# Kernel optimization log

Hardware: AMD Instinct MI355X
Metric: run time of the kernel (lower is better)

The kernel has to match this reference:

```python
import jax, jax.numpy as jnp
from jax import lax
import numpy as np

DIM = 48
HEADS = 2
HIDDEN = 96  # int(dim * 2.0)
EPS_LN = 1e-5
EPS_NORM = 1e-12


def _ln(x, w, b):
    # WithBias LayerNorm over channel dim (dim=1 in NCHW == last dim in b,(hw),c)
    mu = jnp.mean(x, axis=1, keepdims=True)
    var = jnp.var(x, axis=1, keepdims=True)
    return (x - mu) / jnp.sqrt(var + EPS_LN) * w[None, :, None, None] + b[None, :, None, None]


def _conv1x1(x, w, b):
    # w: [O, C, 1, 1]
    return jnp.einsum('bchw,oc->bohw', x, w[:, :, 0, 0]) + b[None, :, None, None]


def _dwconv3(x, w, b):
    # w: [C, 1, 3, 3], groups=C
    y = lax.conv_general_dilated(x, w, (1, 1), 'SAME',
                                 feature_group_count=x.shape[1],
                                 dimension_numbers=('NCHW', 'OIHW', 'NCHW'))
    return y + b[None, :, None, None]


def _l2norm(x):
    n = jnp.sqrt(jnp.sum(x * x, axis=-1, keepdims=True))
    return x / jnp.maximum(n, EPS_NORM)


def setup_inputs() -> dict:
    key = jax.random.key(0)
    ks = jax.random.split(key, 12)
    s = 0.02
    inp = {
        'x': jax.random.normal(ks[0], (2, DIM, 64, 64), jnp.float32),
        'norm1_w': jnp.ones((DIM,), jnp.float32),
        'norm1_b': jnp.zeros((DIM,), jnp.float32),
        'qkv_w': jax.random.normal(ks[1], (DIM * 3, DIM, 1, 1), jnp.float32) * s,
        'qkv_b': jnp.zeros((DIM * 3,), jnp.float32),
        'qkvdw_w': jax.random.normal(ks[2], (DIM * 3, 1, 3, 3), jnp.float32) * s,
        'qkvdw_b': jnp.zeros((DIM * 3,), jnp.float32),
        'temperature': jnp.ones((HEADS, 1, 1), jnp.float32),
        'proj_w': jax.random.normal(ks[3], (DIM, DIM, 1, 1), jnp.float32) * s,
        'proj_b': jnp.zeros((DIM,), jnp.float32),
        'norm2_w': jnp.ones((DIM,), jnp.float32),
        'norm2_b': jnp.zeros((DIM,), jnp.float32),
        'fi_w': jax.random.normal(ks[4], (HIDDEN * 2, DIM, 1, 1), jnp.float32) * s,
        'fi_b': jnp.zeros((HIDDEN * 2,), jnp.float32),
        'fdw_w': jax.random.normal(ks[5], (HIDDEN * 2, 1, 3, 3), jnp.float32) * s,
        'fdw_b': jnp.zeros((HIDDEN * 2,), jnp.float32),
        'fo_w': jax.random.normal(ks[6], (DIM, HIDDEN, 1, 1), jnp.float32) * s,
        'fo_b': jnp.zeros((DIM,), jnp.float32),
    }
    return inp


def _block(x, norm1_w, norm1_b, qkv_w, qkv_b, qkvdw_w, qkvdw_b, temperature,
           proj_w, proj_b, norm2_w, norm2_b, fi_w, fi_b, fdw_w, fdw_b, fo_w, fo_b):
    b, c, h, w = x.shape
    n = h * w
    chead = c // HEADS
    # --- attention branch ---
    xn = _ln(x, norm1_w, norm1_b)
    qkv = _dwconv3(_conv1x1(xn, qkv_w, qkv_b), qkvdw_w, qkvdw_b)
    q, k, v = jnp.split(qkv, 3, axis=1)
    def to_heads(t):  # [b, heads*chead, h, w] -> [b, heads, n, chead]
        return t.reshape(b, HEADS, chead, n).transpose(0, 1, 3, 2)
    q, k, v = to_heads(q), to_heads(k), to_heads(v)
    q = _l2norm(q)
    k = _l2norm(k)
    attn = jnp.einsum('bhnc,bhmc->bhnm', q, k) * temperature[None]
    attn = jax.nn.softmax(attn, axis=-1)
    out = jnp.einsum('bhnm,bhmc->bhnc', attn, v)
    out = out.transpose(0, 1, 3, 2).reshape(b, c, h, w)
    x = x + _conv1x1(out, proj_w, proj_b)
    # --- ffn branch ---
    xn = _ln(x, norm2_w, norm2_b)
    y = _dwconv3(_conv1x1(xn, fi_w, fi_b), fdw_w, fdw_b)
    y1, y2 = jnp.split(y, 2, axis=1)
    y = jax.nn.gelu(y1, approximate=False) * y2
    x = x + _conv1x1(y, fo_w, fo_b)
    return x


def reference(x, norm1_w, norm1_b, qkv_w, qkv_b, qkvdw_w, qkvdw_b, temperature,
              proj_w, proj_b, norm2_w, norm2_b, fi_w, fi_b, fdw_w, fdw_b, fo_w, fo_b):
    return _block(x, norm1_w, norm1_b, qkv_w, qkv_b, qkvdw_w, qkvdw_b, temperature,
                  proj_w, proj_b, norm2_w, norm2_b, fi_w, fi_b, fdw_w, fdw_b, fo_w, fo_b)
```

## Files before the change

kernel.cpp:

```cpp
#include <hip/hip_runtime.h>
#include <hip/hip_bf16.h>
#include <math.h>

#define NPIX 4096
#define NB 2

typedef __attribute__((ext_vector_type(8))) short short8;
typedef __attribute__((ext_vector_type(4))) short short4s;
typedef __attribute__((ext_vector_type(4))) float floatx4;

static __device__ inline short f2bf(float f) {
    union { float f; unsigned u; } v; v.f = f;
    unsigned r = (v.u + 0x7FFFu + ((v.u >> 16) & 1u)) >> 16;
    return (short)r;
}
static __device__ inline float bf2f(short s) {
    union { unsigned u; float f; } v;
    v.u = ((unsigned)(unsigned short)s) << 16;
    return v.f;
}
static __device__ inline unsigned pk2(float a, float b) {
    __hip_bfloat162 pk = __float22bfloat162_rn(make_float2(a, b));
    return *(unsigned*)&pk;
}

__global__ void k_prepw(const float* __restrict__ qkvw, const float* __restrict__ fiw,
                        const float* __restrict__ fow, const float* __restrict__ projw,
                        short* __restrict__ qkvwbf, short* __restrict__ fiwbf,
                        short* __restrict__ fowbf, short* __restrict__ projwbf) {
    int idx = blockIdx.x * 256 + threadIdx.x;
    if (idx < 144 * 64) {
        int o = idx >> 6, c = idx & 63;
        qkvwbf[idx] = (c < 48) ? f2bf(qkvw[o * 48 + c]) : (short)0;
        return;
    }
    idx -= 144 * 64;
    if (idx < 192 * 64) {
        int o = idx >> 6, c = idx & 63;
        fiwbf[idx] = (c < 48) ? f2bf(fiw[o * 48 + c]) : (short)0;
        return;
    }
    idx -= 192 * 64;
    if (idx < 48 * 96) {
        fowbf[idx] = f2bf(fow[idx]);
        return;
    }
    idx -= 48 * 96;
    if (idx < 48 * 64) {
        int o = idx >> 6, c = idx & 63;
        int h = c >> 5, cc = c & 31;
        projwbf[idx] = (cc < 24) ? f2bf(projw[o * 48 + h * 24 + cc]) : (short)0;
    }
}

__global__ __launch_bounds__(256) void k_qkv_fused(
    const float* __restrict__ xin, const float* __restrict__ n1w, const float* __restrict__ n1b,
    const short* __restrict__ qkvwbf, const float* __restrict__ qkvb,
    const float* __restrict__ dww, const float* __restrict__ dwb,
    const float* __restrict__ temp,
    short* __restrict__ Qbf, short* __restrict__ Kbf, short* __restrict__ Vbf)
{
    int px0 = blockIdx.x * 16;
    int y = blockIdx.y, b = blockIdx.z;
    int t = threadIdx.x;
    int w = t >> 6, lane = t & 63, l15 = lane & 15, quad = lane >> 4;

    __shared__ __align__(16) short xn[64][72];
    __shared__ short qkv[64][148];
    __shared__ float q2[16][148];
    __shared__ float red[4][64], redq[4][64];
    __shared__ float muS[64], rsS[64];
    __shared__ float dwwS[1296], dwbS[144];
    __shared__ short vmask[64];

    for (int u = t; u < 1296; u += 256) dwwS[u] = dww[u];
    if (t < 144) dwbS[t] = dwb[t];

    int pp = t & 63, cg = t >> 6;
    int rr = pp / 18, ix = pp - rr * 18;
    int yy = y + rr - 1, xpx = px0 - 1 + ix;
    bool pv = (pp < 54) && ((unsigned)yy < 64u) && ((unsigned)xpx < 64u);
    if (cg == 0) vmask[pp] = pv ? (short)1 : (short)0;

    float v[12]; float s = 0.f, sq = 0.f;
    if (pv) {
        size_t pbase = (size_t)(yy * 64 + xpx);
#pragma unroll
        for (int j = 0; j < 12; j++) {
            float vv = xin[((size_t)b * 48 + cg * 12 + j) * NPIX + pbase];
            v[j] = vv; s += vv; sq += vv * vv;
        }
    } else {
#pragma unroll
        for (int j = 0; j < 12; j++) v[j] = 0.f;
    }
    red[cg][pp] = s; redq[cg][pp] = sq;
    __syncthreads();
    if (t < 64) {
        float ss = red[0][t] + red[1][t] + red[2][t] + red[3][t];
        float qq = redq[0][t] + redq[1][t] + redq[2][t] + redq[3][t];
        float mu = ss * (1.f / 48.f);
        float var = qq * (1.f / 48.f) - mu * mu;
        muS[t] = mu; rsS[t] = rsqrtf(var + 1e-5f);
    }
    __syncthreads();
    {
        float mu = muS[pp], rs = rsS[pp];
#pragma unroll
        for (int j = 0; j < 12; j++) {
            int c = cg * 12 + j;
            xn[pp][c] = f2bf((v[j] - mu) * rs * n1w[c] + n1b[c]);
        }
        short8 z8 = {};
        if (cg == 0) *(short8*)&xn[pp][48] = z8;
        else if (cg == 1) *(short8*)&xn[pp][56] = z8;
    }
    __syncthreads();
    floatx4 zf = {0.f, 0.f, 0.f, 0.f};
    for (int job = w; job < 36; job += 4) {
        int pt = job / 9, ot = job % 9;
        short8 a0 = *(const short8*)&xn[pt * 16 + l15][quad * 8];
        short8 a1 = *(const short8*)&xn[pt * 16 + l15][32 + quad * 8];
        const short* wb = qkvwbf + (ot * 16 + l15) * 64;
        short8 b0 = *(const short8*)(wb + quad * 8);
        short8 b1 = *(const short8*)(wb + 32 + quad * 8);
        floatx4 c = __builtin_amdgcn_mfma_f32_16x16x32_bf16(a0, b0, zf, 0, 0, 0);
        c = __builtin_amdgcn_mfma_f32_16x16x32_bf16(a1, b1, c, 0, 0, 0);
        int oc = ot * 16 + l15;
        float bi = qkvb[oc];
#pragma unroll
        for (int r = 0; r < 4; r++) {
            int opp = pt * 16 + quad * 4 + r;
            qkv[opp][oc] = vmask[opp] ? f2bf(c[r] + bi) : (short)0;
        }
    }
    __syncthreads();
    {
        int i = t & 15, g = t >> 4;
        for (int cc = 0; cc < 9; cc++) {
            int c = g * 9 + cc;
            const float* wp = dwwS + c * 9;
            float acc = dwbS[c];
#pragma unroll
            for (int dy = 0; dy < 3; dy++)
#pragma unroll
                for (int dx = 0; dx < 3; dx++)
                    acc += bf2f(qkv[dy * 18 + i + dx][c]) * wp[dy * 3 + dx];
            q2[i][c] = acc;
        }
    }
    __syncthreads();
    if (t < 128) {
        int i = t & 15, h = (t >> 4) & 1, sel = t >> 5;
        int n = y * 64 + px0 + i;
        int bh = b * 2 + h;
        if (sel < 2) {
            float vv2[24]; float ss = 0.f;
            int base = sel * 48 + h * 24;
#pragma unroll
            for (int c = 0; c < 24; c++) { vv2[c] = q2[i][base + c]; ss += vv2[c] * vv2[c]; }
            float sc = ((sel == 0) ? temp[h] : 1.f) / fmaxf(sqrtf(ss), 1e-12f);
            short qs[32];
#pragma unroll
            for (int c = 0; c < 24; c++) qs[c] = f2bf(vv2[c] * sc);
#pragma unroll
            for (int c = 24; c < 32; c++) qs[c] = 0;
            short* dst = ((sel == 0) ? Qbf : Kbf) + ((size_t)bh * NPIX + n) * 32;
#pragma unroll
            for (int i8 = 0; i8 < 4; i8++) {
                short8 st;
#pragma unroll
                for (int j = 0; j < 8; j++) st[j] = qs[i8 * 8 + j];
                *(short8*)(dst + i8 * 8) = st;
            }
        } else {
            int half = sel - 2;
            int r5 = n & 31;
            int pos = (r5 < 16) ? ((r5 >> 2) * 8 + (r5 & 3))
                                : (((r5 & 15) >> 2) * 8 + (r5 & 3) + 4);
            int vcol = (n & ~31) + pos;
#pragma unroll
            for (int cc = 0; cc < 12; cc++) {
                int c = half * 12 + cc;
                Vbf[((size_t)bh * 32 + c) * NPIX + vcol] = f2bf(q2[i][96 + h * 24 + c]);
            }
            if (half == 1) {
#pragma unroll
                for (int c = 24; c < 32; c++)
                    Vbf[((size_t)bh * 32 + c) * NPIX + vcol] = 0;
            }
        }
    }
}

__global__ __launch_bounds__(1024) void k_attn_mfma2(
    const short* __restrict__ Qbf, const short* __restrict__ Kbf,
    const short* __restrict__ Vbf, short* __restrict__ O)
{
    int qt = blockIdx.x, bh = blockIdx.y;
    int t = threadIdx.x;
    int tg = t & 255, g = t >> 8;
    int wloc = (t >> 6) & 3, lane = t & 63, l15 = lane & 15, quad = lane >> 4;

    __shared__ __align__(16) short tileK[4][2][64][40];
    __shared__ __align__(16) short tileV[4][2][32][72];
    __shared__ float Ocomb[4][64][33];
    __shared__ float Lcomb[4][64];

    int qrow0 = qt * 64 + wloc * 16;
    short8 bq = *(const short8*)(Qbf + ((size_t)bh * NPIX + qrow0 + l15) * 32 + quad * 8);

    int krow = tg >> 2, kseg = tg & 3;
    int vch = tg >> 3, vseg = tg & 7;
    const short* srcK = Kbf + ((size_t)bh * NPIX + krow) * 32 + kseg * 8;
    const short* srcV = Vbf + ((size_t)(bh * 32 + vch)) * NPIX + vseg * 8;

    int key0 = g * 1024;
    *(short8*)&tileK[g][0][krow][kseg * 8] = *(const short8*)(srcK + (size_t)key0 * 32);
    *(short8*)&tileV[g][0][vch][vseg * 8]  = *(const short8*)(srcV + key0);

    floatx4 zf = {0.f, 0.f, 0.f, 0.f};
    floatx4 o0 = zf, o1 = zf;
    float ls = 0.f;

    const int NKT = 16;
    for (int kt = 0; kt < NKT; kt++) {
        __syncthreads();
        int cur = kt & 1;
        short8 ldK = {}, ldV = {};
        if (kt < NKT - 1) {
            int kabs = key0 + (kt + 1) * 64;
            ldK = *(const short8*)(srcK + (size_t)kabs * 32);
            ldV = *(const short8*)(srcV + kabs);
        }
        short8 ka0 = *(const short8*)&tileK[g][cur][l15][quad * 8];
        short8 ka1 = *(const short8*)&tileK[g][cur][16 + l15][quad * 8];
        short8 ka2 = *(const short8*)&tileK[g][cur][32 + l15][quad * 8];
        short8 ka3 = *(const short8*)&tileK[g][cur][48 + l15][quad * 8];
        floatx4 s0 = __builtin_amdgcn_mfma_f32_16x16x32_bf16(ka0, bq, zf, 0, 0, 0);
        floatx4 s1 = __builtin_amdgcn_mfma_f32_16x16x32_bf16(ka1, bq, zf, 0, 0, 0);
        floatx4 s2 = __builtin_amdgcn_mfma_f32_16x16x32_bf16(ka2, bq, zf, 0, 0, 0);
        floatx4 s3 = __builtin_amdgcn_mfma_f32_16x16x32_bf16(ka3, bq, zf, 0, 0, 0);
        float e0[4], e1[4], e2[4], e3[4];
#pragma unroll
        for (int r = 0; r < 4; r++) {
            e0[r] = __expf(s0[r]); e1[r] = __expf(s1[r]);
            e2[r] = __expf(s2[r]); e3[r] = __expf(s3[r]);
            ls += (e0[r] + e1[r]) + (e2[r] + e3[r]);
        }
        short8 p01, p23;
        {
            unsigned* u01 = (unsigned*)&p01;
            unsigned* u23 = (unsigned*)&p23;
            u01[0] = pk2(e0[0], e0[1]); u01[1] = pk2(e0[2], e0[3]);
            u01[2] = pk2(e1[0], e1[1]); u01[3] = pk2(e1[2], e1[3]);
            u23[0] = pk2(e2[0], e2[1]); u23[1] = pk2(e2[2], e2[3]);
            u23[2] = pk2(e3[0], e3[1]); u23[3] = pk2(e3[2], e3[3]);
        }
        short8 va00 = *(const short8*)&tileV[g][cur][l15][quad * 8];
        short8 va01 = *(const short8*)&tileV[g][cur][l15][32 + quad * 8];
        short8 va10 = *(const short8*)&tileV[g][cur][16 + l15][quad * 8];
        short8 va11 = *(const short8*)&tileV[g][cur][16 + l15][32 + quad * 8];
        o0 = __builtin_amdgcn_mfma_f32_16x16x32_bf16(va00, p01, o0, 0, 0, 0);
        o0 = __builtin_amdgcn_mfma_f32_16x16x32_bf16(va01, p23, o0, 0, 0, 0);
        o1 = __builtin_amdgcn_mfma_f32_16x16x32_bf16(va10, p01, o1, 0, 0, 0);
        o1 = __builtin_amdgcn_mfma_f32_16x16x32_bf16(va11, p23, o1, 0, 0, 0);
        if (kt < NKT - 1) {
            *(short8*)&tileK[g][1 - cur][krow][kseg * 8] = ldK;
            *(short8*)&tileV[g][1 - cur][vch][vseg * 8]  = ldV;
        }
    }
    ls += __shfl_xor(ls, 16, 64);
    ls += __shfl_xor(ls, 32, 64);
    int qi = wloc * 16 + l15;
#pragma unroll
    for (int r = 0; r < 4; r++) {
        Ocomb[g][qi][quad * 4 + r]      = o0[r];
        Ocomb[g][qi][16 + quad * 4 + r] = o1[r];
    }
    if (quad == 0) Lcomb[g][qi] = ls;
    __syncthreads();
    {
        int qq = t >> 4, cp = t & 15;
        float l4 = Lcomb[0][qq] + Lcomb[1][qq] + Lcomb[2][qq] + Lcomb[3][qq];
        float inv = 1.f / l4;
        float sa = (Ocomb[0][qq][2 * cp] + Ocomb[1][qq][2 * cp] +
                    Ocomb[2][qq][2 * cp] + Ocomb[3][qq][2 * cp]) * inv;
        float sb = (Ocomb[0][qq][2 * cp + 1] + Ocomb[1][qq][2 * cp + 1] +
                    Ocomb[2][qq][2 * cp + 1] + Ocomb[3][qq][2 * cp + 1]) * inv;
        int b = bh >> 1, h = bh & 1;
        int n = qt * 64 + qq;
        *(unsigned*)(O + ((size_t)b * NPIX + n) * 64 + h * 32 + 2 * cp) = pk2(sa, sb);
    }
}

__global__ __launch_bounds__(256) void k_tail_fused(
    const float* __restrict__ xin, const short* __restrict__ O,
    const short* __restrict__ projwbf, const float* __restrict__ projb,
    const float* __restrict__ n2w, const float* __restrict__ n2b,
    const short* __restrict__ fiwbf, const float* __restrict__ fib,
    const float* __restrict__ fdww, const float* __restrict__ fdwb,
    const short* __restrict__ fowbf, const float* __restrict__ fob,
    float* __restrict__ out)
{
    int px0 = blockIdx.x * 16;
    int y = blockIdx.y, b = blockIdx.z;
    int t = threadIdx.x;
    int w = t >> 6, lane = t & 63, l15 = lane & 15, quad = lane >> 4;

    __shared__ float x1s[64][53];
    __shared__ __align__(16) short xn2[64][72];
    __shared__ short ypre[56][196];
    __shared__ __align__(16) short yv[16][104];
    __shared__ float red[4][64], redq[4][64];
    __shared__ float muS[64], rsS[64];
    __shared__ float fdwwS[1728], fdwbS[192];
    __shared__ short vmask[64];
    __shared__ int nidx[64];

    for (int u = t; u < 1728; u += 256) fdwwS[u] = fdww[u];
    if (t < 192) fdwbS[t] = fdwb[t];
    if (t < 64) {
        int rr = t / 18, ix = t - rr * 18;
        int yy = y + rr - 1, xpx = px0 - 1 + ix;
        bool pv = (t < 54) && ((unsigned)yy < 64u) && ((unsigned)xpx < 64u);
        vmask[t] = pv ? (short)1 : (short)0;
        int n = yy * 64 + xpx;
        n = n < 0 ? 0 : (n > 4095 ? 4095 : n);
        nidx[t] = n;
    }
    __syncthreads();

    floatx4 zf = {0.f, 0.f, 0.f, 0.f};
    for (int job = w; job < 12; job += 4) {
        int pt = job / 3, ot = job % 3;
        const short* oa = O + ((size_t)b * NPIX + nidx[pt * 16 + l15]) * 64;
        short8 a0 = *(const short8*)(oa + quad * 8);
        short8 a1 = *(const short8*)(oa + 32 + quad * 8);
        const short* wb = projwbf + (ot * 16 + l15) * 64;
        short8 b0 = *(const short8*)(wb + quad * 8);
        short8 b1 = *(const short8*)(wb + 32 + quad * 8);
        floatx4 c = __builtin_amdgcn_mfma_f32_16x16x32_bf16(a0, b0, zf, 0, 0, 0);
        c = __builtin_amdgcn_mfma_f32_16x16x32_bf16(a1, b1, c, 0, 0, 0);
        int oc = ot * 16 + l15;
        float bi = projb[oc];
#pragma unroll
        for (int r = 0; r < 4; r++) {
            int opp = pt * 16 + quad * 4 + r;
            x1s[opp][oc] = xin[((size_t)b * 48 + oc) * NPIX + nidx[opp]] + c[r] + bi;
        }
    }
    __syncthreads();
    int pp = t & 63, cg = t >> 6;
    {
        float v[12]; float s = 0.f, sq = 0.f;
#pragma unroll
        for (int j = 0; j < 12; j++) {
            float vv = x1s[pp][cg * 12 + j];
            v[j] = vv; s += vv; sq += vv * vv;
        }
        red[cg][pp] = s; redq[cg][pp] = sq;
        __syncthreads();
        if (t < 64) {
            float ss = red[0][t] + red[1][t] + red[2][t] + red[3][t];
            float qq = redq[0][t] + redq[1][t] + redq[2][t] + redq[3][t];
            float mu = ss * (1.f / 48.f);
            float var = qq * (1.f / 48.f) - mu * mu;
            muS[t] = mu; rsS[t] = rsqrtf(var + 1e-5f);
        }
        __syncthreads();
        float mu = muS[pp], rs = rsS[pp];
#pragma unroll
        for (int j = 0; j < 12; j++) {
            int c = cg * 12 + j;
            xn2[pp][c] = f2bf((v[j] - mu) * rs * n2w[c] + n2b[c]);
        }
        short8 z8 = {};
        if (cg == 0) *(short8*)&xn2[pp][48] = z8;
        else if (cg == 1) *(short8*)&xn2[pp][56] = z8;
    }
    __syncthreads();
    for (int job = w; job < 48; job += 4) {
        int pt = job / 12, ot = job % 12;
        short8 a0 = *(const short8*)&xn2[pt * 16 + l15][quad * 8];
        short8 a1 = *(const short8*)&xn2[pt * 16 + l15][32 + quad * 8];
        const short* wb = fiwbf + (ot * 16 + l15) * 64;
        short8 b0 = *(const short8*)(wb + quad * 8);
        short8 b1 = *(const short8*)(wb + 32 + quad * 8);
        floatx4 c = __builtin_amdgcn_mfma_f32_16x16x32_bf16(a0, b0, zf, 0, 0, 0);
        c = __builtin_amdgcn_mfma_f32_16x16x32_bf16(a1, b1, c, 0, 0, 0);
        int oc = ot * 16 + l15;
        float bi = fib[oc];
#pragma unroll
        for (int r = 0; r < 4; r++) {
            int opp = pt * 16 + quad * 4 + r;
            if (opp < 56) ypre[opp][oc] = vmask[opp] ? f2bf(c[r] + bi) : (short)0;
        }
    }
    __syncthreads();
    {
        int i = t & 15, gg = t >> 4;
        for (int cc = 0; cc < 6; cc++) {
            int c = gg * 6 + cc;
            const float* wp  = fdwwS + c * 9;
            const float* wp2 = fdwwS + (c + 96) * 9;
            float a = fdwbS[c], g2v = fdwbS[c + 96];
#pragma unroll
            for (int dy = 0; dy < 3; dy++)
#pragma unroll
                for (int dx = 0; dx < 3; dx++) {
                    int ppi = dy * 18 + i + dx;
                    a   += bf2f(ypre[ppi][c])      * wp[dy * 3 + dx];
                    g2v += bf2f(ypre[ppi][c + 96]) * wp2[dy * 3 + dx];
                }
            float ge = 0.5f * a * (1.f + erff(a * 0.70710678118654752f));
            yv[i][c] = f2bf(ge * g2v);
        }
        short8 z8 = {};
        if (gg == 0) *(short8*)&yv[i][96] = z8;
    }
    __syncthreads();
    if (w < 3) {
        floatx4 c = zf;
#pragma unroll
        for (int k = 0; k < 3; k++) {
            short8 a  = *(const short8*)&yv[l15][k * 32 + quad * 8];
            short8 bb = *(const short8*)(fowbf + (w * 16 + l15) * 96 + k * 32 + quad * 8);
            c = __builtin_amdgcn_mfma_f32_16x16x32_bf16(a, bb, c, 0, 0, 0);
        }
        int oc = w * 16 + l15;
        float bi = fob[oc];
#pragma unroll
        for (int r = 0; r < 4; r++) {
            int i = quad * 4 + r;
            size_t idx = ((size_t)b * 48 + oc) * NPIX + y * 64 + px0 + i;
            out[idx] = x1s[19 + i][oc] + c[r] + bi;
        }
    }
}

extern "C" void kernel_launch(void* const* d_in, const int* in_sizes, int n_in,
                              void* d_out, int out_size, void* d_ws, size_t ws_size,
                              hipStream_t stream) {
    const float* x       = (const float*)d_in[0];
    const float* n1w     = (const float*)d_in[1];
    const float* n1b     = (const float*)d_in[2];
    const float* qkv_w   = (const float*)d_in[3];
    const float* qkv_b   = (const float*)d_in[4];
    const float* qkvdw_w = (const float*)d_in[5];
    const float* qkvdw_b = (const float*)d_in[6];
    const float* temp    = (const float*)d_in[7];
    const float* proj_w  = (const float*)d_in[8];
    const float* proj_b  = (const float*)d_in[9];
    const float* n2w     = (const float*)d_in[10];
    const float* n2b     = (const float*)d_in[11];
    const float* fi_w    = (const float*)d_in[12];
    const float* fi_b    = (const float*)d_in[13];
    const float* fdw_w   = (const float*)d_in[14];
    const float* fdw_b   = (const float*)d_in[15];
    const float* fo_w    = (const float*)d_in[16];
    const float* fo_b    = (const float*)d_in[17];

    short* sws = (short*)d_ws;
    short* Qbf     = sws;
    short* Kbf     = Qbf + 524288;
    short* Vbf     = Kbf + 524288;
    short* Obuf    = Vbf + 524288;
    short* qkvwbf  = Obuf + 524288;
    short* fiwbf   = qkvwbf + 9216;
    short* fowbf   = fiwbf + 12288;
    short* projwbf = fowbf + 4608;

    {
        int total = 144 * 64 + 192 * 64 + 48 * 96 + 48 * 64;
        k_prepw<<<(total + 255) / 256, 256, 0, stream>>>(qkv_w, fi_w, fo_w, proj_w,
                                                         qkvwbf, fiwbf, fowbf, projwbf);
    }
    {
        dim3 g(4, 64, NB);
        k_qkv_fused<<<g, 256, 0, stream>>>(x, n1w, n1b, qkvwbf, qkv_b,
                                           qkvdw_w, qkvdw_b, temp, Qbf, Kbf, Vbf);
    }
    {
        dim3 g(64, 4);
        k_attn_mfma2<<<g, 1024, 0, stream>>>(Qbf, Kbf, Vbf, Obuf);
    }
    {
        dim3 g(4, 64, NB);
        k_tail_fused<<<g, 256, 0, stream>>>(x, Obuf, projwbf, proj_b, n2w, n2b,
                                            fiwbf, fi_b, fdw_w, fdw_b, fowbf, fo_b,
                                            (float*)d_out);
    }
}
```

Baseline: 139.5 us.

## Merge all stages into one cooperative persistent kernel with grid syncs

Replaces the four separate launches (weight prep, qkv, attention, tail) with a single cooperative kernel of 512 blocks that runs the phases in order, separated by grid-wide barriers. Weight conversion is folded into phase 0, and the qkv weights are staged straight into shared memory. Shared memory is unioned across phases. The aim is to remove launch gaps and the extra prep kernel. In exchange, attention now runs on 512 blocks of 256 threads instead of 256 blocks of 1024, and grid syncs add their own cost. If the cooperative launch fails, it falls back to three ordinary launches.

```diff
diff --git a/kernel.cpp b/kernel.cpp
--- a/kernel.cpp
+++ b/kernel.cpp
@@ -1,6 +1,9 @@
 #include <hip/hip_runtime.h>
+#include <hip/hip_cooperative_groups.h>
 #include <hip/hip_bf16.h>
 #include <math.h>
+
+namespace cg = cooperative_groups;
 
 #define NPIX 4096
 #define NB 2
@@ -24,417 +27,425 @@
     return *(unsigned*)&pk;
 }
 
-__global__ void k_prepw(const float* __restrict__ qkvw, const float* __restrict__ fiw,
-                        const float* __restrict__ fow, const float* __restrict__ projw,
-                        short* __restrict__ qkvwbf, short* __restrict__ fiwbf,
-                        short* __restrict__ fowbf, short* __restrict__ projwbf) {
-    int idx = blockIdx.x * 256 + threadIdx.x;
-    if (idx < 144 * 64) {
-        int o = idx >> 6, c = idx & 63;
-        qkvwbf[idx] = (c < 48) ? f2bf(qkvw[o * 48 + c]) : (short)0;
-        return;
-    }
-    idx -= 144 * 64;
-    if (idx < 192 * 64) {
-        int o = idx >> 6, c = idx & 63;
-        fiwbf[idx] = (c < 48) ? f2bf(fiw[o * 48 + c]) : (short)0;
-        return;
-    }
-    idx -= 192 * 64;
-    if (idx < 48 * 96) {
-        fowbf[idx] = f2bf(fow[idx]);
-        return;
-    }
-    idx -= 48 * 96;
-    if (idx < 48 * 64) {
-        int o = idx >> 6, c = idx & 63;
-        int h = c >> 5, cc = c & 31;
-        projwbf[idx] = (cc < 24) ? f2bf(projw[o * 48 + h * 24 + cc]) : (short)0;
-    }
-}
-
-__global__ __launch_bounds__(256) void k_qkv_fused(
-    const float* __restrict__ xin, const float* __restrict__ n1w, const float* __restrict__ n1b,
-    const short* __restrict__ qkvwbf, const float* __restrict__ qkvb,
+struct SA_t {
+    short xn[64][72];
+    short qkv[64][148];
+    union {
+        short wA[144][72];
+        struct { float q2[16][148]; float dwwS[1296]; float dwbS[144]; } d;
+    } u;
+    float red[4][64], redq[4][64];
+    float muS[64], rsS[64];
+    short vmask[64];
+};
+struct SB_t {
+    float Ocomb[4][32][33];
+    float Lcomb[4][32];
+};
+struct SC_t {
+    float x1s[64][53];
+    short xn2[64][72];
+    short ypre[56][196];
+    short yv[16][104];
+    float red[4][64], redq[4][64];
+    float muS[64], rsS[64];
+    float fdwwS[1728], fdwbS[192];
+    short vmask[64];
+    int nidx[64];
+};
+union SU_t { SA_t a; SB_t b; SC_t c; };
+
+__global__ __launch_bounds__(256, 2) void k_mega(
+    int phase,
+    const float* __restrict__ xin,
+    const float* __restrict__ n1w, const float* __restrict__ n1b,
+    const float* __restrict__ qkvw, const float* __restrict__ qkvb,
     const float* __restrict__ dww, const float* __restrict__ dwb,
     const float* __restrict__ temp,
-    short* __restrict__ Qbf, short* __restrict__ Kbf, short* __restrict__ Vbf)
-{
-    int px0 = blockIdx.x * 16;
-    int y = blockIdx.y, b = blockIdx.z;
-    int t = threadIdx.x;
-    int w = t >> 6, lane = t & 63, l15 = lane & 15, quad = lane >> 4;
-
-    __shared__ __align__(16) short xn[64][72];
-    __shared__ short qkv[64][148];
-    __shared__ float q2[16][148];
-    __shared__ float red[4][64], redq[4][64];
-    __shared__ float muS[64], rsS[64];
-    __shared__ float dwwS[1296], dwbS[144];
-    __shared__ short vmask[64];
-
-    for (int u = t; u < 1296; u += 256) dwwS[u] = dww[u];
-    if (t < 144) dwbS[t] = dwb[t];
-
-    int pp = t & 63, cg = t >> 6;
-    int rr = pp / 18, ix = pp - rr * 18;
-    int yy = y + rr - 1, xpx = px0 - 1 + ix;
-    bool pv = (pp < 54) && ((unsigned)yy < 64u) && ((unsigned)xpx < 64u);
-    if (cg == 0) vmask[pp] = pv ? (short)1 : (short)0;
-
-    float v[12]; float s = 0.f, sq = 0.f;
-    if (pv) {
-        size_t pbase = (size_t)(yy * 64 + xpx);
-#pragma unroll
-        for (int j = 0; j < 12; j++) {
-            float vv = xin[((size_t)b * 48 + cg * 12 + j) * NPIX + pbase];
-            v[j] = vv; s += vv; sq += vv * vv;
-        }
-    } else {
-#pragma unroll
-        for (int j = 0; j < 12; j++) v[j] = 0.f;
-    }
-    red[cg][pp] = s; redq[cg][pp] = sq;
-    __syncthreads();
-    if (t < 64) {
-        float ss = red[0][t] + red[1][t] + red[2][t] + red[3][t];
-        float qq = redq[0][t] + redq[1][t] + redq[2][t] + redq[3][t];
-        float mu = ss * (1.f / 48.f);
-        float var = qq * (1.f / 48.f) - mu * mu;
-        muS[t] = mu; rsS[t] = rsqrtf(var + 1e-5f);
-    }
-    __syncthreads();
-    {
-        float mu = muS[pp], rs = rsS[pp];
-#pragma unroll
-        for (int j = 0; j < 12; j++) {
-            int c = cg * 12 + j;
-            xn[pp][c] = f2bf((v[j] - mu) * rs * n1w[c] + n1b[c]);
-        }
-        short8 z8 = {};
-        if (cg == 0) *(short8*)&xn[pp][48] = z8;
-        else if (cg == 1) *(short8*)&xn[pp][56] = z8;
-    }
-    __syncthreads();
-    floatx4 zf = {0.f, 0.f, 0.f, 0.f};
-    for (int job = w; job < 36; job += 4) {
-        int pt = job / 9, ot = job % 9;
-        short8 a0 = *(const short8*)&xn[pt * 16 + l15][quad * 8];
-        short8 a1 = *(const short8*)&xn[pt * 16 + l15][32 + quad * 8];
-        const short* wb = qkvwbf + (ot * 16 + l15) * 64;
-        short8 b0 = *(const short8*)(wb + quad * 8);
-        short8 b1 = *(const short8*)(wb + 32 + quad * 8);
-        floatx4 c = __builtin_amdgcn_mfma_f32_16x16x32_bf16(a0, b0, zf, 0, 0, 0);
-        c = __builtin_amdgcn_mfma_f32_16x16x32_bf16(a1, b1, c, 0, 0, 0);
-        int oc = ot * 16 + l15;
-        float bi = qkvb[oc];
-#pragma unroll
-        for (int r = 0; r < 4; r++) {
-            int opp = pt * 16 + quad * 4 + r;
-            qkv[opp][oc] = vmask[opp] ? f2bf(c[r] + bi) : (short)0;
-        }
-    }
-    __syncthreads();
-    {
-        int i = t & 15, g = t >> 4;
-        for (int cc = 0; cc < 9; cc++) {
-            int c = g * 9 + cc;
-            const float* wp = dwwS + c * 9;
-            float acc = dwbS[c];
-#pragma unroll
-            for (int dy = 0; dy < 3; dy++)
-#pragma unroll
-                for (int dx = 0; dx < 3; dx++)
-                    acc += bf2f(qkv[dy * 18 + i + dx][c]) * wp[dy * 3 + dx];
-            q2[i][c] = acc;
-        }
-    }
-    __syncthreads();
-    if (t < 128) {
-        int i = t & 15, h = (t >> 4) & 1, sel = t >> 5;
-        int n = y * 64 + px0 + i;
-        int bh = b * 2 + h;
-        if (sel < 2) {
-            float vv2[24]; float ss = 0.f;
-            int base = sel * 48 + h * 24;
-#pragma unroll
-            for (int c = 0; c < 24; c++) { vv2[c] = q2[i][base + c]; ss += vv2[c] * vv2[c]; }
-            float sc = ((sel == 0) ? temp[h] : 1.f) / fmaxf(sqrtf(ss), 1e-12f);
-            short qs[32];
-#pragma unroll
-            for (int c = 0; c < 24; c++) qs[c] = f2bf(vv2[c] * sc);
-#pragma unroll
-            for (int c = 24; c < 32; c++) qs[c] = 0;
-            short* dst = ((sel == 0) ? Qbf : Kbf) + ((size_t)bh * NPIX + n) * 32;
-#pragma unroll
-            for (int i8 = 0; i8 < 4; i8++) {
-                short8 st;
-#pragma unroll
-                for (int j = 0; j < 8; j++) st[j] = qs[i8 * 8 + j];
-                *(short8*)(dst + i8 * 8) = st;
-            }
-        } else {
-            int half = sel - 2;
-            int r5 = n & 31;
-            int pos = (r5 < 16) ? ((r5 >> 2) * 8 + (r5 & 3))
-                                : (((r5 & 15) >> 2) * 8 + (r5 & 3) + 4);
-            int vcol = (n & ~31) + pos;
-#pragma unroll
-            for (int cc = 0; cc < 12; cc++) {
-                int c = half * 12 + cc;
-                Vbf[((size_t)bh * 32 + c) * NPIX + vcol] = f2bf(q2[i][96 + h * 24 + c]);
-            }
-            if (half == 1) {
-#pragma unroll
-                for (int c = 24; c < 32; c++)
-                    Vbf[((size_t)bh * 32 + c) * NPIX + vcol] = 0;
-            }
-        }
-    }
-}
-
-__global__ __launch_bounds__(1024) void k_attn_mfma2(
-    const short* __restrict__ Qbf, const short* __restrict__ Kbf,
-    const short* __restrict__ Vbf, short* __restrict__ O)
-{
-    int qt = blockIdx.x, bh = blockIdx.y;
-    int t = threadIdx.x;
-    int tg = t & 255, g = t >> 8;
-    int wloc = (t >> 6) & 3, lane = t & 63, l15 = lane & 15, quad = lane >> 4;
-
-    __shared__ __align__(16) short tileK[4][2][64][40];
-    __shared__ __align__(16) short tileV[4][2][32][72];
-    __shared__ float Ocomb[4][64][33];
-    __shared__ float Lcomb[4][64];
-
-    int qrow0 = qt * 64 + wloc * 16;
-    short8 bq = *(const short8*)(Qbf + ((size_t)bh * NPIX + qrow0 + l15) * 32 + quad * 8);
-
-    int krow = tg >> 2, kseg = tg & 3;
-    int vch = tg >> 3, vseg = tg & 7;
-    const short* srcK = Kbf + ((size_t)bh * NPIX + krow) * 32 + kseg * 8;
-    const short* srcV = Vbf + ((size_t)(bh * 32 + vch)) * NPIX + vseg * 8;
-
-    int key0 = g * 1024;
-    *(short8*)&tileK[g][0][krow][kseg * 8] = *(const short8*)(srcK + (size_t)key0 * 32);
-    *(short8*)&tileV[g][0][vch][vseg * 8]  = *(const short8*)(srcV + key0);
-
-    floatx4 zf = {0.f, 0.f, 0.f, 0.f};
-    floatx4 o0 = zf, o1 = zf;
-    float ls = 0.f;
-
-    const int NKT = 16;
-    for (int kt = 0; kt < NKT; kt++) {
-        __syncthreads();
-        int cur = kt & 1;
-        short8 ldK = {}, ldV = {};
-        if (kt < NKT - 1) {
-            int kabs = key0 + (kt + 1) * 64;
-            ldK = *(const short8*)(srcK + (size_t)kabs * 32);
-            ldV = *(const short8*)(srcV + kabs);
-        }
-        short8 ka0 = *(const short8*)&tileK[g][cur][l15][quad * 8];
-        short8 ka1 = *(const short8*)&tileK[g][cur][16 + l15][quad * 8];
-        short8 ka2 = *(const short8*)&tileK[g][cur][32 + l15][quad * 8];
-        short8 ka3 = *(const short8*)&tileK[g][cur][48 + l15][quad * 8];
-        floatx4 s0 = __builtin_amdgcn_mfma_f32_16x16x32_bf16(ka0, bq, zf, 0, 0, 0);
-        floatx4 s1 = __builtin_amdgcn_mfma_f32_16x16x32_bf16(ka1, bq, zf, 0, 0, 0);
-        floatx4 s2 = __builtin_amdgcn_mfma_f32_16x16x32_bf16(ka2, bq, zf, 0, 0, 0);
-        floatx4 s3 = __builtin_amdgcn_mfma_f32_16x16x32_bf16(ka3, bq, zf, 0, 0, 0);
-        float e0[4], e1[4], e2[4], e3[4];
-#pragma unroll
-        for (int r = 0; r < 4; r++) {
-            e0[r] = __expf(s0[r]); e1[r] = __expf(s1[r]);
-            e2[r] = __expf(s2[r]); e3[r] = __expf(s3[r]);
-            ls += (e0[r] + e1[r]) + (e2[r] + e3[r]);
-        }
-        short8 p01, p23;
-        {
-            unsigned* u01 = (unsigned*)&p01;
-            unsigned* u23 = (unsigned*)&p23;
-            u01[0] = pk2(e0[0], e0[1]); u01[1] = pk2(e0[2], e0[3]);
-            u01[2] = pk2(e1[0], e1[1]); u01[3] = pk2(e1[2], e1[3]);
-            u23[0] = pk2(e2[0], e2[1]); u23[1] = pk2(e2[2], e2[3]);
-            u23[2] = pk2(e3[0], e3[1]); u23[3] = pk2(e3[2], e3[3]);
-        }
-        short8 va00 = *(const short8*)&tileV[g][cur][l15][quad * 8];
-        short8 va01 = *(const short8*)&tileV[g][cur][l15][32 + quad * 8];
-        short8 va10 = *(const short8*)&tileV[g][cur][16 + l15][quad * 8];
-        short8 va11 = *(const short8*)&tileV[g][cur][16 + l15][32 + quad * 8];
-        o0 = __builtin_amdgcn_mfma_f32_16x16x32_bf16(va00, p01, o0, 0, 0, 0);
-        o0 = __builtin_amdgcn_mfma_f32_16x16x32_bf16(va01, p23, o0, 0, 0, 0);
-        o1 = __builtin_amdgcn_mfma_f32_16x16x32_bf16(va10, p01, o1, 0, 0, 0);
-        o1 = __builtin_amdgcn_mfma_f32_16x16x32_bf16(va11, p23, o1, 0, 0, 0);
-        if (kt < NKT - 1) {
-            *(short8*)&tileK[g][1 - cur][krow][kseg * 8] = ldK;
-            *(short8*)&tileV[g][1 - cur][vch][vseg * 8]  = ldV;
-        }
-    }
-    ls += __shfl_xor(ls, 16, 64);
-    ls += __shfl_xor(ls, 32, 64);
-    int qi = wloc * 16 + l15;
-#pragma unroll
-    for (int r = 0; r < 4; r++) {
-        Ocomb[g][qi][quad * 4 + r]      = o0[r];
-        Ocomb[g][qi][16 + quad * 4 + r] = o1[r];
-    }
-    if (quad == 0) Lcomb[g][qi] = ls;
-    __syncthreads();
-    {
-        int qq = t >> 4, cp = t & 15;
-        float l4 = Lcomb[0][qq] + Lcomb[1][qq] + Lcomb[2][qq] + Lcomb[3][qq];
-        float inv = 1.f / l4;
-        float sa = (Ocomb[0][qq][2 * cp] + Ocomb[1][qq][2 * cp] +
-                    Ocomb[2][qq][2 * cp] + Ocomb[3][qq][2 * cp]) * inv;
-        float sb = (Ocomb[0][qq][2 * cp + 1] + Ocomb[1][qq][2 * cp + 1] +
-                    Ocomb[2][qq][2 * cp + 1] + Ocomb[3][qq][2 * cp + 1]) * inv;
-        int b = bh >> 1, h = bh & 1;
-        int n = qt * 64 + qq;
-        *(unsigned*)(O + ((size_t)b * NPIX + n) * 64 + h * 32 + 2 * cp) = pk2(sa, sb);
-    }
-}
-
-__global__ __launch_bounds__(256) void k_tail_fused(
-    const float* __restrict__ xin, const short* __restrict__ O,
-    const short* __restrict__ projwbf, const float* __restrict__ projb,
+    const float* __restrict__ projw, const float* __restrict__ projb,
     const float* __restrict__ n2w, const float* __restrict__ n2b,
-    const short* __restrict__ fiwbf, const float* __restrict__ fib,
+    const float* __restrict__ fiw, const float* __restrict__ fib,
     const float* __restrict__ fdww, const float* __restrict__ fdwb,
-    const short* __restrict__ fowbf, const float* __restrict__ fob,
+    const float* __restrict__ fow, const float* __restrict__ fob,
+    short* __restrict__ Qbf, short* __restrict__ Kbf, short* __restrict__ Vbf,
+    short* __restrict__ Obuf,
+    short* __restrict__ fiwbf, short* __restrict__ fowbf, short* __restrict__ projwbf,
     float* __restrict__ out)
 {
-    int px0 = blockIdx.x * 16;
-    int y = blockIdx.y, b = blockIdx.z;
+    __shared__ __align__(16) SU_t sm;
     int t = threadIdx.x;
+    int bid = blockIdx.x;
     int w = t >> 6, lane = t & 63, l15 = lane & 15, quad = lane >> 4;
-
-    __shared__ float x1s[64][53];
-    __shared__ __align__(16) short xn2[64][72];
-    __shared__ short ypre[56][196];
-    __shared__ __align__(16) short yv[16][104];
-    __shared__ float red[4][64], redq[4][64];
-    __shared__ float muS[64], rsS[64];
-    __shared__ float fdwwS[1728], fdwbS[192];
-    __shared__ short vmask[64];
-    __shared__ int nidx[64];
-
-    for (int u = t; u < 1728; u += 256) fdwwS[u] = fdww[u];
-    if (t < 192) fdwbS[t] = fdwb[t];
-    if (t < 64) {
-        int rr = t / 18, ix = t - rr * 18;
+    floatx4 zf = {0.f, 0.f, 0.f, 0.f};
+    bool all = (phase < 0);
+
+    if (all || phase == 0) {
+        int px0 = (bid & 3) * 16;
+        int y = (bid >> 2) & 63;
+        int b = bid >> 8;
+        {
+            int gt = bid * 256 + t;
+            if (gt < 12288) {
+                int o = gt >> 6, c = gt & 63;
+                fiwbf[gt] = (c < 48) ? f2bf(fiw[o * 48 + c]) : (short)0;
+            } else if (gt < 16896) {
+                int u2 = gt - 12288;
+                fowbf[u2] = f2bf(fow[u2]);
+            } else if (gt < 19968) {
+                int u2 = gt - 16896;
+                int o = u2 >> 6, c = u2 & 63;
+                int h = c >> 5, cc = c & 31;
+                projwbf[u2] = (cc < 24) ? f2bf(projw[o * 48 + h * 24 + cc]) : (short)0;
+            }
+        }
+        for (int u2 = t; u2 < 144 * 64; u2 += 256) {
+            int o = u2 >> 6, c = u2 & 63;
+            sm.a.u.wA[o][c] = (c < 48) ? f2bf(qkvw[o * 48 + c]) : (short)0;
+        }
+        int pp = t & 63, cg2 = t >> 6;
+        int rr = pp / 18, ix = pp - rr * 18;
         int yy = y + rr - 1, xpx = px0 - 1 + ix;
-        bool pv = (t < 54) && ((unsigned)yy < 64u) && ((unsigned)xpx < 64u);
-        vmask[t] = pv ? (short)1 : (short)0;
-        int n = yy * 64 + xpx;
-        n = n < 0 ? 0 : (n > 4095 ? 4095 : n);
-        nidx[t] = n;
-    }
-    __syncthreads();
-
-    floatx4 zf = {0.f, 0.f, 0.f, 0.f};
-    for (int job = w; job < 12; job += 4) {
-        int pt = job / 3, ot = job % 3;
-        const short* oa = O + ((size_t)b * NPIX + nidx[pt * 16 + l15]) * 64;
-        short8 a0 = *(const short8*)(oa + quad * 8);
-        short8 a1 = *(const short8*)(oa + 32 + quad * 8);
-        const short* wb = projwbf + (ot * 16 + l15) * 64;
-        short8 b0 = *(const short8*)(wb + quad * 8);
-        short8 b1 = *(const short8*)(wb + 32 + quad * 8);
-        floatx4 c = __builtin_amdgcn_mfma_f32_16x16x32_bf16(a0, b0, zf, 0, 0, 0);
-        c = __builtin_amdgcn_mfma_f32_16x16x32_bf16(a1, b1, c, 0, 0, 0);
-        int oc = ot * 16 + l15;
-        float bi = projb[oc];
-#pragma unroll
-        for (int r = 0; r < 4; r++) {
-            int opp = pt * 16 + quad * 4 + r;
-            x1s[opp][oc] = xin[((size_t)b * 48 + oc) * NPIX + nidx[opp]] + c[r] + bi;
-        }
-    }
-    __syncthreads();
-    int pp = t & 63, cg = t >> 6;
-    {
+        bool pv = (pp < 54) && ((unsigned)yy < 64u) && ((unsigned)xpx < 64u);
+        if (cg2 == 0) sm.a.vmask[pp] = pv ? (short)1 : (short)0;
         float v[12]; float s = 0.f, sq = 0.f;
-#pragma unroll
-        for (int j = 0; j < 12; j++) {
-            float vv = x1s[pp][cg * 12 + j];
-            v[j] = vv; s += vv; sq += vv * vv;
-        }
-        red[cg][pp] = s; redq[cg][pp] = sq;
+        if (pv) {
+            size_t pbase = (size_t)(yy * 64 + xpx);
+#pragma unroll
+            for (int j2 = 0; j2 < 12; j2++) {
+                float vv = xin[((size_t)b * 48 + cg2 * 12 + j2) * NPIX + pbase];
+                v[j2] = vv; s += vv; sq += vv * vv;
+            }
+        } else {
+#pragma unroll
+            for (int j2 = 0; j2 < 12; j2++) v[j2] = 0.f;
+        }
+        sm.a.red[cg2][pp] = s; sm.a.redq[cg2][pp] = sq;
         __syncthreads();
         if (t < 64) {
-            float ss = red[0][t] + red[1][t] + red[2][t] + red[3][t];
-            float qq = redq[0][t] + redq[1][t] + redq[2][t] + redq[3][t];
+            float ss = sm.a.red[0][t] + sm.a.red[1][t] + sm.a.red[2][t] + sm.a.red[3][t];
+            float qq = sm.a.redq[0][t] + sm.a.redq[1][t] + sm.a.redq[2][t] + sm.a.redq[3][t];
             float mu = ss * (1.f / 48.f);
             float var = qq * (1.f / 48.f) - mu * mu;
-            muS[t] = mu; rsS[t] = rsqrtf(var + 1e-5f);
-        }
-        __syncthreads();
-        float mu = muS[pp], rs = rsS[pp];
-#pragma unroll
-        for (int j = 0; j < 12; j++) {
-            int c = cg * 12 + j;
-            xn2[pp][c] = f2bf((v[j] - mu) * rs * n2w[c] + n2b[c]);
-        }
-        short8 z8 = {};
-        if (cg == 0) *(short8*)&xn2[pp][48] = z8;
-        else if (cg == 1) *(short8*)&xn2[pp][56] = z8;
+            sm.a.muS[t] = mu; sm.a.rsS[t] = rsqrtf(var + 1e-5f);
+        }
+        __syncthreads();
+        {
+            float mu = sm.a.muS[pp], rs = sm.a.rsS[pp];
+#pragma unroll
+            for (int j2 = 0; j2 < 12; j2++) {
+                int c = cg2 * 12 + j2;
+                sm.a.xn[pp][c] = f2bf((v[j2] - mu) * rs * n1w[c] + n1b[c]);
+            }
+            short8 z8 = {};
+            if (cg2 == 0) *(short8*)&sm.a.xn[pp][48] = z8;
+            else if (cg2 == 1) *(short8*)&sm.a.xn[pp][56] = z8;
+        }
+        __syncthreads();
+        for (int job = w; job < 36; job += 4) {
+            int pt = job / 9, ot = job % 9;
+            short8 a0 = *(const short8*)&sm.a.xn[pt * 16 + l15][quad * 8];
+            short8 a1 = *(const short8*)&sm.a.xn[pt * 16 + l15][32 + quad * 8];
+            const short* wb = &sm.a.u.wA[ot * 16 + l15][0];
+            short8 b0 = *(const short8*)(wb + quad * 8);
+            short8 b1 = *(const short8*)(wb + 32 + quad * 8);
+            floatx4 c = __builtin_amdgcn_mfma_f32_16x16x32_bf16(a0, b0, zf, 0, 0, 0);
+            c = __builtin_amdgcn_mfma_f32_16x16x32_bf16(a1, b1, c, 0, 0, 0);
+            int oc = ot * 16 + l15;
+            float bi = qkvb[oc];
+#pragma unroll
+            for (int r = 0; r < 4; r++) {
+                int opp = pt * 16 + quad * 4 + r;
+                sm.a.qkv[opp][oc] = sm.a.vmask[opp] ? f2bf(c[r] + bi) : (short)0;
+            }
+        }
+        __syncthreads();
+        for (int u2 = t; u2 < 1296; u2 += 256) sm.a.u.d.dwwS[u2] = dww[u2];
+        if (t < 144) sm.a.u.d.dwbS[t] = dwb[t];
+        __syncthreads();
+        {
+            int i = t & 15, g3 = t >> 4;
+            for (int cc = 0; cc < 9; cc++) {
+                int c = g3 * 9 + cc;
+                const float* wp = sm.a.u.d.dwwS + c * 9;
+                float acc = sm.a.u.d.dwbS[c];
+#pragma unroll
+                for (int dy = 0; dy < 3; dy++)
+#pragma unroll
+                    for (int dx = 0; dx < 3; dx++)
+                        acc += bf2f(sm.a.qkv[dy * 18 + i + dx][c]) * wp[dy * 3 + dx];
+                sm.a.u.d.q2[i][c] = acc;
+            }
+        }
+        __syncthreads();
+        if (t < 128) {
+            int i = t & 15, h = (t >> 4) & 1, sel = t >> 5;
+            int n = y * 64 + px0 + i;
+            int bh = b * 2 + h;
+            if (sel < 2) {
+                float vv2[24]; float ss = 0.f;
+                int base = sel * 48 + h * 24;
+#pragma unroll
+                for (int c = 0; c < 24; c++) { vv2[c] = sm.a.u.d.q2[i][base + c]; ss += vv2[c] * vv2[c]; }
+                float sc = ((sel == 0) ? temp[h] * 1.44269504089f : 1.f) / fmaxf(sqrtf(ss), 1e-12f);
+                short qs[32];
+#pragma unroll
+                for (int c = 0; c < 24; c++) qs[c] = f2bf(vv2[c] * sc);
+#pragma unroll
+                for (int c = 24; c < 32; c++) qs[c] = 0;
+                short* dst = ((sel == 0) ? Qbf : Kbf) + ((size_t)bh * NPIX + n) * 32;
+#pragma unroll
+                for (int i8 = 0; i8 < 4; i8++) {
+                    short8 st;
+#pragma unroll
+                    for (int j2 = 0; j2 < 8; j2++) st[j2] = qs[i8 * 8 + j2];
+                    *(short8*)(dst + i8 * 8) = st;
+                }
+            } else {
+                int half = sel - 2;
+                int r5 = n & 31;
+                int pos = (r5 < 16) ? ((r5 >> 2) * 8 + (r5 & 3))
+                                    : (((r5 & 15) >> 2) * 8 + (r5 & 3) + 4);
+                int vcol = (n & ~31) + pos;
+#pragma unroll
+                for (int cc = 0; cc < 12; cc++) {
+                    int c = half * 12 + cc;
+                    Vbf[((size_t)bh * 32 + c) * NPIX + vcol] = f2bf(sm.a.u.d.q2[i][96 + h * 24 + c]);
+                }
+                if (half == 1) {
+#pragma unroll
+                    for (int c = 24; c < 32; c++)
+                        Vbf[((size_t)bh * 32 + c) * NPIX + vcol] = 0;
+                }
+            }
+        }
     }
-    __syncthreads();
-    for (int job = w; job < 48; job += 4) {
-        int pt = job / 12, ot = job % 12;
-        short8 a0 = *(const short8*)&xn2[pt * 16 + l15][quad * 8];
-        short8 a1 = *(const short8*)&xn2[pt * 16 + l15][32 + quad * 8];
-        const short* wb = fiwbf + (ot * 16 + l15) * 64;
-        short8 b0 = *(const short8*)(wb + quad * 8);
-        short8 b1 = *(const short8*)(wb + 32 + quad * 8);
-        floatx4 c = __builtin_amdgcn_mfma_f32_16x16x32_bf16(a0, b0, zf, 0, 0, 0);
-        c = __builtin_amdgcn_mfma_f32_16x16x32_bf16(a1, b1, c, 0, 0, 0);
-        int oc = ot * 16 + l15;
-        float bi = fib[oc];
+
+    if (all) cg::this_grid().sync();
+
+    if (all || phase == 1) {
+        int qt32 = bid >> 2, bh = bid & 3;
+        int qrow0 = qt32 * 32;
+        short8 bq0 = *(const short8*)(Qbf + ((size_t)bh * NPIX + qrow0 + l15) * 32 + quad * 8);
+        short8 bq1 = *(const short8*)(Qbf + ((size_t)bh * NPIX + qrow0 + 16 + l15) * 32 + quad * 8);
+        const short* Kb = Kbf + (size_t)bh * NPIX * 32;
+        const short* Vb = Vbf + (size_t)bh * 32 * NPIX;
+        floatx4 o00 = zf, o01 = zf, o10 = zf, o11 = zf;
+        float ls0 = 0.f, ls1 = 0.f;
+        int key0 = w * 1024;
+        for (int kt = 0; kt < 16; kt++) {
+            int kabs = key0 + kt * 64;
+            short8 ka0 = *(const short8*)(Kb + (size_t)(kabs + l15) * 32 + quad * 8);
+            short8 ka1 = *(const short8*)(Kb + (size_t)(kabs + 16 + l15) * 32 + quad * 8);
+            short8 ka2 = *(const short8*)(Kb + (size_t)(kabs + 32 + l15) * 32 + quad * 8);
+            short8 ka3 = *(const short8*)(Kb + (size_t)(kabs + 48 + l15) * 32 + quad * 8);
+            short8 va00 = *(const short8*)(Vb + (size_t)l15 * NPIX + kabs + quad * 8);
+            short8 va01 = *(const short8*)(Vb + (size_t)l15 * NPIX + kabs + 32 + quad * 8);
+            short8 va10 = *(const short8*)(Vb + (size_t)(16 + l15) * NPIX + kabs + quad * 8);
+            short8 va11 = *(const short8*)(Vb + (size_t)(16 + l15) * NPIX + kabs + 32 + quad * 8);
+            {
+                floatx4 s0 = __builtin_amdgcn_mfma_f32_16x16x32_bf16(ka0, bq0, zf, 0, 0, 0);
+                floatx4 s1 = __builtin_amdgcn_mfma_f32_16x16x32_bf16(ka1, bq0, zf, 0, 0, 0);
+                floatx4 s2 = __builtin_amdgcn_mfma_f32_16x16x32_bf16(ka2, bq0, zf, 0, 0, 0);
+                floatx4 s3 = __builtin_amdgcn_mfma_f32_16x16x32_bf16(ka3, bq0, zf, 0, 0, 0);
+                float e0[4], e1[4], e2[4], e3[4];
+#pragma unroll
+                for (int r = 0; r < 4; r++) {
+                    e0[r] = exp2f(s0[r]); e1[r] = exp2f(s1[r]);
+                    e2[r] = exp2f(s2[r]); e3[r] = exp2f(s3[r]);
+                    ls0 += (e0[r] + e1[r]) + (e2[r] + e3[r]);
+                }
+                short8 p01, p23;
+                unsigned* u01 = (unsigned*)&p01;
+                unsigned* u23 = (unsigned*)&p23;
+                u01[0] = pk2(e0[0], e0[1]); u01[1] = pk2(e0[2], e0[3]);
+                u01[2] = pk2(e1[0], e1[1]); u01[3] = pk2(e1[2], e1[3]);
+                u23[0] = pk2(e2[0], e2[1]); u23[1] = pk2(e2[2], e2[3]);
+                u23[2] = pk2(e3[0], e3[1]); u23[3] = pk2(e3[2], e3[3]);
+                o00 = __builtin_amdgcn_mfma_f32_16x16x32_bf16(va00, p01, o00, 0, 0, 0);
+                o00 = __builtin_amdgcn_mfma_f32_16x16x32_bf16(va01, p23, o00, 0, 0, 0);
+                o01 = __builtin_amdgcn_mfma_f32_16x16x32_bf16(va10, p01, o01, 0, 0, 0);
+                o01 = __builtin_amdgcn_mfma_f32_16x16x32_bf16(va11, p23, o01, 0, 0, 0);
+            }
+            {
+                floatx4 s0 = __builtin_amdgcn_mfma_f32_16x16x32_bf16(ka0, bq1, zf, 0, 0, 0);
+                floatx4 s1 = __builtin_amdgcn_mfma_f32_16x16x32_bf16(ka1, bq1, zf, 0, 0, 0);
+                floatx4 s2 = __builtin_amdgcn_mfma_f32_16x16x32_bf16(ka2, bq1, zf, 0, 0, 0);
+                floatx4 s3 = __builtin_amdgcn_mfma_f32_16x16x32_bf16(ka3, bq1, zf, 0, 0, 0);
+                float e0[4], e1[4], e2[4], e3[4];
+#pragma unroll
+                for (int r = 0; r < 4; r++) {
+                    e0[r] = exp2f(s0[r]); e1[r] = exp2f(s1[r]);
+                    e2[r] = exp2f(s2[r]); e3[r] = exp2f(s3[r]);
+                    ls1 += (e0[r] + e1[r]) + (e2[r] + e3[r]);
+                }
+                short8 p01, p23;
+                unsigned* u01 = (unsigned*)&p01;
+                unsigned* u23 = (unsigned*)&p23;
+                u01[0] = pk2(e0[0], e0[1]); u01[1] = pk2(e0[2], e0[3]);
+                u01[2] = pk2(e1[0], e1[1]); u01[3] = pk2(e1[2], e1[3]);
+                u23[0] = pk2(e2[0], e2[1]); u23[1] = pk2(e2[2], e2[3]);
+                u23[2] = pk2(e3[0], e3[1]); u23[3] = pk2(e3[2], e3[3]);
+                o10 = __builtin_amdgcn_mfma_f32_16x16x32_bf16(va00, p01, o10, 0, 0, 0);
+                o10 = __builtin_amdgcn_mfma_f32_16x16x32_bf16(va01, p23, o10, 0, 0, 0);
+                o11 = __builtin_amdgcn_mfma_f32_16x16x32_bf16(va10, p01, o11, 0, 0, 0);
+                o11 = __builtin_amdgcn_mfma_f32_16x16x32_bf16(va11, p23, o11, 0, 0, 0);
+            }
+        }
+        ls0 += __shfl_xor(ls0, 16, 64); ls0 += __shfl_xor(ls0, 32, 64);
+        ls1 += __shfl_xor(ls1, 16, 64); ls1 += __shfl_xor(ls1, 32, 64);
+        __syncthreads();
 #pragma unroll
         for (int r = 0; r < 4; r++) {
-            int opp = pt * 16 + quad * 4 + r;
-            if (opp < 56) ypre[opp][oc] = vmask[opp] ? f2bf(c[r] + bi) : (short)0;
+            sm.b.Ocomb[w][l15][quad * 4 + r]           = o00[r];
+            sm.b.Ocomb[w][l15][16 + quad * 4 + r]      = o01[r];
+            sm.b.Ocomb[w][16 + l15][quad * 4 + r]      = o10[r];
+            sm.b.Ocomb[w][16 + l15][16 + quad * 4 + r] = o11[r];
+        }
+        if (quad == 0) { sm.b.Lcomb[w][l15] = ls0; sm.b.Lcomb[w][16 + l15] = ls1; }
+        __syncthreads();
+        {
+            int qq = t >> 3, cp0 = t & 7;
+            float l4 = sm.b.Lcomb[0][qq] + sm.b.Lcomb[1][qq] +
+                       sm.b.Lcomb[2][qq] + sm.b.Lcomb[3][qq];
+            float inv = 1.f / l4;
+            int b2 = bh >> 1, h = bh & 1;
+            int n = qrow0 + qq;
+#pragma unroll
+            for (int half = 0; half < 2; half++) {
+                int cp = cp0 + half * 8;
+                float sa2 = (sm.b.Ocomb[0][qq][2 * cp] + sm.b.Ocomb[1][qq][2 * cp] +
+                             sm.b.Ocomb[2][qq][2 * cp] + sm.b.Ocomb[3][qq][2 * cp]) * inv;
+                float sb2 = (sm.b.Ocomb[0][qq][2 * cp + 1] + sm.b.Ocomb[1][qq][2 * cp + 1] +
+                             sm.b.Ocomb[2][qq][2 * cp + 1] + sm.b.Ocomb[3][qq][2 * cp + 1]) * inv;
+                *(unsigned*)(Obuf + ((size_t)b2 * NPIX + n) * 64 + h * 32 + 2 * cp) = pk2(sa2, sb2);
+            }
         }
     }
-    __syncthreads();
-    {
-        int i = t & 15, gg = t >> 4;
-        for (int cc = 0; cc < 6; cc++) {
-            int c = gg * 6 + cc;
-            const float* wp  = fdwwS + c * 9;
-            const float* wp2 = fdwwS + (c + 96) * 9;
-            float a = fdwbS[c], g2v = fdwbS[c + 96];
-#pragma unroll
-            for (int dy = 0; dy < 3; dy++)
-#pragma unroll
-                for (int dx = 0; dx < 3; dx++) {
-                    int ppi = dy * 18 + i + dx;
-                    a   += bf2f(ypre[ppi][c])      * wp[dy * 3 + dx];
-                    g2v += bf2f(ypre[ppi][c + 96]) * wp2[dy * 3 + dx];
-                }
-            float ge = 0.5f * a * (1.f + erff(a * 0.70710678118654752f));
-            yv[i][c] = f2bf(ge * g2v);
-        }
-        short8 z8 = {};
-        if (gg == 0) *(short8*)&yv[i][96] = z8;
-    }
-    __syncthreads();
-    if (w < 3) {
-        floatx4 c = zf;
-#pragma unroll
-        for (int k = 0; k < 3; k++) {
-            short8 a  = *(const short8*)&yv[l15][k * 32 + quad * 8];
-            short8 bb = *(const short8*)(fowbf + (w * 16 + l15) * 96 + k * 32 + quad * 8);
-            c = __builtin_amdgcn_mfma_f32_16x16x32_bf16(a, bb, c, 0, 0, 0);
-        }
-        int oc = w * 16 + l15;
-        float bi = fob[oc];
-#pragma unroll
-        for (int r = 0; r < 4; r++) {
-            int i = quad * 4 + r;
-            size_t idx = ((size_t)b * 48 + oc) * NPIX + y * 64 + px0 + i;
-            out[idx] = x1s[19 + i][oc] + c[r] + bi;
+
+    if (all) cg::this_grid().sync();
+
+    if (all || phase == 2) {
+        int px0 = (bid & 3) * 16;
+        int y = (bid >> 2) & 63;
+        int b = bid >> 8;
+
+        for (int u2 = t; u2 < 1728; u2 += 256) sm.c.fdwwS[u2] = fdww[u2];
+        if (t < 192) sm.c.fdwbS[t] = fdwb[t];
+        if (t < 64) {
+            int rr = t / 18, ix = t - rr * 18;
+            int yy = y + rr - 1, xpx = px0 - 1 + ix;
+            bool pv = (t < 54) && ((unsigned)yy < 64u) && ((unsigned)xpx < 64u);
+            sm.c.vmask[t] = pv ? (short)1 : (short)0;
+            int n = yy * 64 + xpx;
+            n = n < 0 ? 0 : (n > 4095 ? 4095 : n);
+            sm.c.nidx[t] = n;
+        }
+        __syncthreads();
+
+        for (int job = w; job < 12; job += 4) {
+            int pt = job / 3, ot = job % 3;
+            const short* oa = Obuf + ((size_t)b * NPIX + sm.c.nidx[pt * 16 + l15]) * 64;
+            short8 a0 = *(const short8*)(oa + quad * 8);
+            short8 a1 = *(const short8*)(oa + 32 + quad * 8);
+            const short* wb = projwbf + (ot * 16 + l15) * 64;
+            short8 b0 = *(const short8*)(wb + quad * 8);
+            short8 b1 = *(const short8*)(wb + 32 + quad * 8);
+            floatx4 c = __builtin_amdgcn_mfma_f32_16x16x32_bf16(a0, b0, zf, 0, 0, 0);
+            c = __builtin_amdgcn_mfma_f32_16x16x32_bf16(a1, b1, c, 0, 0, 0);
+            int oc = ot * 16 + l15;
+            float bi = projb[oc];
+#pragma unroll
+            for (int r = 0; r < 4; r++) {
+                int opp = pt * 16 + quad * 4 + r;
+                sm.c.x1s[opp][oc] = xin[((size_t)b * 48 + oc) * NPIX + sm.c.nidx[opp]] + c[r] + bi;
+            }
+        }
+        __syncthreads();
+        int pp = t & 63, cg2 = t >> 6;
+        {
+            float v[12]; float s = 0.f, sq = 0.f;
+#pragma unroll
+            for (int j2 = 0; j2 < 12; j2++) {
+                float vv = sm.c.x1s[pp][cg2 * 12 + j2];
+                v[j2] = vv; s += vv; sq += vv * vv;
+            }
+            sm.c.red[cg2][pp] = s; sm.c.redq[cg2][pp] = sq;
+            __syncthreads();
+            if (t < 64) {
+                float ss = sm.c.red[0][t] + sm.c.red[1][t] + sm.c.red[2][t] + sm.c.red[3][t];
+                float qq = sm.c.redq[0][t] + sm.c.redq[1][t] + sm.c.redq[2][t] + sm.c.redq[3][t];
+                float mu = ss * (1.f / 48.f);
+                float var = qq * (1.f / 48.f) - mu * mu;
+                sm.c.muS[t] = mu; sm.c.rsS[t] = rsqrtf(var + 1e-5f);
+            }
+            __syncthreads();
+            float mu = sm.c.muS[pp], rs = sm.c.rsS[pp];
+#pragma unroll
+            for (int j2 = 0; j2 < 12; j2++) {
+                int c = cg2 * 12 + j2;
+                sm.c.xn2[pp][c] = f2bf((v[j2] - mu) * rs * n2w[c] + n2b[c]);
+            }
+            short8 z8 = {};
+            if (cg2 == 0) *(short8*)&sm.c.xn2[pp][48] = z8;
+            else if (cg2 == 1) *(short8*)&sm.c.xn2[pp][56] = z8;
+        }
+        __syncthreads();
+        for (int job = w; job < 48; job += 4) {
+            int pt = job / 12, ot = job % 12;
+            short8 a0 = *(const short8*)&sm.c.xn2[pt * 16 + l15][quad * 8];
+            short8 a1 = *(const short8*)&sm.c.xn2[pt * 16 + l15][32 + quad * 8];
+            const short* wb = fiwbf + (ot * 16 + l15) * 64;
+            short8 b0 = *(const short8*)(wb + quad * 8);
+            short8 b1 = *(const short8*)(wb + 32 + quad * 8);
+            floatx4 c = __builtin_amdgcn_mfma_f32_16x16x32_bf16(a0, b0, zf, 0, 0, 0);
+            c = __builtin_amdgcn_mfma_f32_16x16x32_bf16(a1, b1, c, 0, 0, 0);
+            int oc = ot * 16 + l15;
+            float bi = fib[oc];
+#pragma unroll
+            for (int r = 0; r < 4; r++) {
+                int opp = pt * 16 + quad * 4 + r;
+                if (opp < 56) sm.c.ypre[opp][oc] = sm.c.vmask[opp] ? f2bf(c[r] + bi) : (short)0;
+            }
+        }
+        __syncthreads();
+        {
+            int i = t & 15, gg = t >> 4;
+            for (int cc = 0; cc < 6; cc++) {
+                int c = gg * 6 + cc;
+                const float* wp  = sm.c.fdwwS + c * 9;
+                const float* wp2 = sm.c.fdwwS + (c + 96) * 9;
+                float a = sm.c.fdwbS[c], g2v = sm.c.fdwbS[c + 96];
+#pragma unroll
+                for (int dy = 0; dy < 3; dy++)
+#pragma unroll
+                    for (int dx = 0; dx < 3; dx++) {
+                        int ppi = dy * 18 + i + dx;
+                        a   += bf2f(sm.c.ypre[ppi][c])      * wp[dy * 3 + dx];
+                        g2v += bf2f(sm.c.ypre[ppi][c + 96]) * wp2[dy * 3 + dx];
+                    }
+                float ge = 0.5f * a * (1.f + erff(a * 0.70710678118654752f));
+                sm.c.yv[i][c] = f2bf(ge * g2v);
+            }
+            short8 z8 = {};
+            if (gg == 0) *(short8*)&sm.c.yv[i][96] = z8;
+        }
+        __syncthreads();
+        if (w < 3) {
+            floatx4 c = zf;
+#pragma unroll
+            for (int k = 0; k < 3; k++) {
+                short8 a  = *(const short8*)&sm.c.yv[l15][k * 32 + quad * 8];
+                short8 bb = *(const short8*)(fowbf + (w * 16 + l15) * 96 + k * 32 + quad * 8);
+                c = __builtin_amdgcn_mfma_f32_16x16x32_bf16(a, bb, c, 0, 0, 0);
+            }
+            int oc = w * 16 + l15;
+            float bi = fob[oc];
+#pragma unroll
+            for (int r = 0; r < 4; r++) {
+                int i = quad * 4 + r;
+                size_t idx = ((size_t)b * 48 + oc) * NPIX + y * 64 + px0 + i;
+                out[idx] = sm.c.x1s[19 + i][oc] + c[r] + bi;
+            }
         }
     }
 }
@@ -460,35 +471,28 @@
     const float* fdw_b   = (const float*)d_in[15];
     const float* fo_w    = (const float*)d_in[16];
     const float* fo_b    = (const float*)d_in[17];
+    float* outp = (float*)d_out;
 
     short* sws = (short*)d_ws;
     short* Qbf     = sws;
     short* Kbf     = Qbf + 524288;
     short* Vbf     = Kbf + 524288;
     short* Obuf    = Vbf + 524288;
-    short* qkvwbf  = Obuf + 524288;
-    short* fiwbf   = qkvwbf + 9216;
+    short* fiwbf   = Obuf + 524288;
     short* fowbf   = fiwbf + 12288;
     short* projwbf = fowbf + 4608;
 
-    {
-        int total = 144 * 64 + 192 * 64 + 48 * 96 + 48 * 64;
-        k_prepw<<<(total + 255) / 256, 256, 0, stream>>>(qkv_w, fi_w, fo_w, proj_w,
-                                                         qkvwbf, fiwbf, fowbf, projwbf);
-    }
-    {
-        dim3 g(4, 64, NB);
-        k_qkv_fused<<<g, 256, 0, stream>>>(x, n1w, n1b, qkvwbf, qkv_b,
-                                           qkvdw_w, qkvdw_b, temp, Qbf, Kbf, Vbf);
-    }
-    {
-        dim3 g(64, 4);
-        k_attn_mfma2<<<g, 1024, 0, stream>>>(Qbf, Kbf, Vbf, Obuf);
-    }
-    {
-        dim3 g(4, 64, NB);
-        k_tail_fused<<<g, 256, 0, stream>>>(x, Obuf, projwbf, proj_b, n2w, n2b,
-                                            fiwbf, fi_b, fdw_w, fdw_b, fowbf, fo_b,
-                                            (float*)d_out);
+    int phase = -1;
+    void* args[] = { &phase, &x, &n1w, &n1b, &qkv_w, &qkv_b, &qkvdw_w, &qkvdw_b, &temp,
+                     &proj_w, &proj_b, &n2w, &n2b, &fi_w, &fi_b, &fdw_w, &fdw_b,
+                     &fo_w, &fo_b, &Qbf, &Kbf, &Vbf, &Obuf, &fiwbf, &fowbf, &projwbf, &outp };
+    hipError_t err = hipLaunchCooperativeKernel((const void*)k_mega, dim3(512), dim3(256),
+                                                args, 0u, stream);
+    if (err != hipSuccess) {
+        (void)hipGetLastError();
+        for (int p = 0; p < 3; p++)
+            k_mega<<<dim3(512), dim3(256), 0, stream>>>(p, x, n1w, n1b, qkv_w, qkv_b,
+                qkvdw_w, qkvdw_b, temp, proj_w, proj_b, n2w, n2b, fi_w, fi_b,
+                fdw_w, fdw_b, fo_w, fo_b, Qbf, Kbf, Vbf, Obuf, fiwbf, fowbf, projwbf, outp);
     }
 }
```

Result: slower. 315.5 us (+126.2%).
